# Kernel optimization log

Hardware: AMD Instinct MI355X
Metric: run time of the kernel (lower is better)

The kernel has to match this reference:

```python
import jax, jax.numpy as jnp
import numpy as np

NEG_INF = -10000.0
ALPHA = 0.2      # LeakyReLU slope
EPS = 1e-5       # LayerNorm eps
B, N, D = 8, 2048, 128


def setup_inputs() -> dict:
    key = jax.random.key(0)
    ks = jax.random.split(key, 8)
    x = jax.random.normal(ks[0], (B, N, D), dtype=jnp.float32)
    adj_bool = jax.random.randint(ks[1], (B, N, N), 0, 2, dtype=jnp.int32)
    node_mask = jax.random.randint(ks[2], (B, N), 0, 2, dtype=jnp.int32)
    s = 1.0 / np.sqrt(D)
    W = jax.random.uniform(ks[3], (D, D), jnp.float32, -s, s)    # fc weight (in->out)
    a_l = jax.random.uniform(ks[4], (D,), jnp.float32, -s, s)    # attn_l weight
    a_r = jax.random.uniform(ks[5], (D,), jnp.float32, -s, s)    # attn_r weight
    gamma = jnp.ones((D,), jnp.float32)                          # LayerNorm weight
    beta = jnp.zeros((D,), jnp.float32)                          # LayerNorm bias
    return {"x": x, "adj_bool": adj_bool, "node_mask": node_mask,
            "W": W, "a_l": a_l, "a_r": a_r, "gamma": gamma, "beta": beta}


def reference(x, adj_bool, node_mask, W, a_l, a_r, gamma, beta):
    m = node_mask.astype(x.dtype)[..., None]           # [B,N,1]
    x = x * m
    h = jnp.einsum('bnd,de->bne', x, W)                # [B,N,D]
    e_l = jnp.einsum('bnd,d->bn', h, a_l)              # [B,N]
    e_r = jnp.einsum('bnd,d->bn', h, a_r)              # [B,N]
    e = e_l[:, :, None] + e_r[:, None, :]              # [B,N,N]
    e = jnp.where(e > 0, e, ALPHA * e)                 # LeakyReLU
    pair = (node_mask[:, :, None] * node_mask[:, None, :]) > 0
    allowed = (adj_bool > 0) & pair
    e = jnp.where(allowed, e, NEG_INF)
    attn = jax.nn.softmax(e, axis=-1)                  # finite (NEG_INF fill), nan_to_num is a no-op
    out = jnp.einsum('bij,bjd->bid', attn, h)          # dropout in eval mode = identity
    out = (out + x) * m                                # residual (ind==outd), then node mask
    mu = jnp.mean(out, axis=-1, keepdims=True)
    var = jnp.var(out, axis=-1, keepdims=True)
    out = (out - mu) * jax.lax.rsqrt(var + EPS) * gamma + beta
    return out
```

## Files before the change

kernel.cpp:

```cpp
#include <hip/hip_runtime.h>
#include <stdint.h>


#define BB 8
#define NN 2048
#define DD 128
#define LN_EPS 1e-5f

typedef __attribute__((ext_vector_type(8))) short short8;
typedef __attribute__((ext_vector_type(4))) float f32x4;

__device__ __forceinline__ unsigned pk_bf16(float a, float b) {
    unsigned ua = __float_as_uint(a); ua += 0x7FFFu + ((ua >> 16) & 1u);
    unsigned ub = __float_as_uint(b); ub += 0x7FFFu + ((ub >> 16) & 1u);
    return (ua >> 16) | (ub & 0xFFFF0000u);
}

__global__ __launch_bounds__(256) void wprep_kernel(
    const float* __restrict__ W, unsigned* __restrict__ WT2g)
{
    const int g  = blockIdx.x * 256 + threadIdx.x;
    const int e  = g & 127;
    const int kp = g >> 7;
    const float w0 = W[(size_t)(2 * kp) * DD + e];
    const float w1 = W[(size_t)(2 * kp + 1) * DD + e];
    WT2g[((size_t)(kp >> 2) * 128 + e) * 4 + (kp & 3)] = pk_bf16(w0, w1);
}

__global__ __launch_bounds__(256) void pack_kernel(
    const int* __restrict__ adj, const int* __restrict__ mask,
    unsigned* __restrict__ adjw)
{
    const int t  = threadIdx.x;
    const int w  = t >> 6, ln = t & 63;
    const int r  = blockIdx.x * 4 + w;
    const int b  = r >> 11;
    const int4* arow4 = (const int4*)(adj + (size_t)r * NN);
    const int4* mrow4 = (const int4*)(mask + ((size_t)b << 11));

    unsigned myword = 0;
#pragma unroll
    for (int c = 0; c < 8; ++c) {
        int4 a = arow4[c * 64 + ln];
        int4 m = mrow4[c * 64 + ln];
        unsigned nib = (unsigned)(a.x & m.x & 1)
                     | ((unsigned)(a.y & m.y & 1) << 1)
                     | ((unsigned)(a.z & m.z & 1) << 2)
                     | ((unsigned)(a.w & m.w & 1) << 3);
        unsigned v = nib << ((ln & 7) * 4);
        v |= __shfl_xor(v, 1, 64);
        v |= __shfl_xor(v, 2, 64);
        v |= __shfl_xor(v, 4, 64);
        unsigned got = __shfl(v, (ln & 7) * 8, 64);
        if ((ln >> 3) == c) myword = got;
    }
    adjw[(size_t)r * 64 + ln] = myword;
}

__global__ __launch_bounds__(256) void fc_kernel(
    const float* __restrict__ x, const int* __restrict__ mask,
    const unsigned* __restrict__ WT2g, const float* __restrict__ a_l,
    const float* __restrict__ a_r, unsigned short* __restrict__ hTX,
    float* __restrict__ el, float* __restrict__ er)
{
    __shared__ __align__(16) unsigned char smem[41984];

    const int t   = threadIdx.x;
    const int blk = blockIdx.x;
    const int b   = blk >> 6;
    const int it  = blk & 63;
    const int i0  = it * 32;
    const int half = it & 1;
    const int jt   = it >> 1;

    unsigned short* WT2 = (unsigned short*)smem;
    unsigned* xs2u = (unsigned*)(smem + 32768);
    unsigned* hws  = (unsigned*)(smem + 32768);

    {
        uint4* d = (uint4*)WT2;
        const uint4* s = (const uint4*)WT2g;
#pragma unroll
        for (int k = 0; k < 8; ++k) d[t + 256 * k] = s[t + 256 * k];
    }

    {
#pragma unroll
        for (int s4 = 0; s4 < 4; ++s4) {
            int idx = t + 256 * s4;
            int i = idx >> 5, c4 = idx & 31;
            float4 f = *(const float4*)(x + ((size_t)(b * NN + i0 + i)) * DD
                                          + c4 * 4);
            float mm = (float)mask[b * NN + i0 + i];
            unsigned p0 = pk_bf16(f.x * mm, f.y * mm);
            unsigned p1 = pk_bf16(f.z * mm, f.w * mm);
            unsigned* dst = xs2u + ((size_t)((c4 >> 1) * 32 + i)) * 4
                          + (c4 & 1) * 2;
            dst[0] = p0; dst[1] = p1;
        }
    }
    __syncthreads();

    const int lane = t & 63, w = t >> 6;
    const int row = lane & 15, grp = lane >> 4;

    f32x4 acc[2][2];
#pragma unroll
    for (int mt = 0; mt < 2; ++mt)
#pragma unroll
        for (int nt = 0; nt < 2; ++nt) acc[mt][nt] = (f32x4)0.f;

#pragma unroll
    for (int kk = 0; kk < 4; ++kk) {
        const unsigned short* cb = WT2 + ((size_t)(kk * 4 + grp) * 128) * 8;
        short8 A0 = *(const short8*)(cb + (w * 32 + row) * 8);
        short8 A1 = *(const short8*)(cb + (w * 32 + 16 + row) * 8);
        const unsigned short* xb = (const unsigned short*)xs2u
                                 + ((size_t)(kk * 4 + grp) * 32) * 8;
#pragma unroll
        for (int nt = 0; nt < 2; ++nt) {
            short8 Bv = *(const short8*)(xb + (nt * 16 + row) * 8);
            acc[0][nt] = __builtin_amdgcn_mfma_f32_16x16x32_bf16(A0, Bv, acc[0][nt], 0, 0, 0);
            acc[1][nt] = __builtin_amdgcn_mfma_f32_16x16x32_bf16(A1, Bv, acc[1][nt], 0, 0, 0);
        }
    }
    __syncthreads();

    float al8[2][4], ar8[2][4];
#pragma unroll
    for (int mt = 0; mt < 2; ++mt)
#pragma unroll
        for (int reg = 0; reg < 4; ++reg) {
            int e = w * 32 + mt * 16 + grp * 4 + reg;
            al8[mt][reg] = a_l[e];
            ar8[mt][reg] = a_r[e];
        }
    float* sE = (float*)smem;
#pragma unroll
    for (int nt = 0; nt < 2; ++nt) {
        float pl = 0.f, pr = 0.f;
#pragma unroll
        for (int mt = 0; mt < 2; ++mt)
#pragma unroll
            for (int reg = 0; reg < 4; ++reg) {
                pl += acc[mt][nt][reg] * al8[mt][reg];
                pr += acc[mt][nt][reg] * ar8[mt][reg];
            }
        pl += __shfl_xor(pl, 16, 64); pl += __shfl_xor(pl, 32, 64);
        pr += __shfl_xor(pr, 16, 64); pr += __shfl_xor(pr, 32, 64);
        if (grp == 0) {
            sE[w * 32 + nt * 16 + row]       = pl;
            sE[128 + w * 32 + nt * 16 + row] = pr;
        }
    }

    unsigned* hw = hws + w * 576;
#pragma unroll
    for (int mt = 0; mt < 2; ++mt)
#pragma unroll
        for (int nt = 0; nt < 2; ++nt)
#pragma unroll
            for (int reg = 0; reg < 4; ++reg) {
                float v  = acc[mt][nt][reg];
                float vp = __shfl_xor(v, 1, 64);
                if ((row & 1) == 0)
                    hw[(mt * 16 + grp * 4 + reg) * 18 + ((nt * 16 + row) >> 1)] =
                        pk_bf16(v, vp);
            }
    {
        const int dl = lane & 31, part = lane >> 5;
        unsigned short* dstb = hTX + (size_t)b * (DD * NN) + (size_t)jt * 8192;
#pragma unroll
        for (int pp = 0; pp < 2; ++pp) {
            int ic2 = part * 2 + pp;
            uint4 q = *(const uint4*)(hw + dl * 18 + ic2 * 4);
            *(uint4*)(dstb + ((size_t)((half * 4 + ic2) * 128 + w * 32 + dl)) * 8) = q;
        }
    }

    __syncthreads();
    if (t < 32)
        el[b * NN + i0 + t] = sE[t] + sE[32 + t] + sE[64 + t] + sE[96 + t];
    else if (t < 64) {
        int i = t - 32;
        er[b * NN + i0 + i] = sE[128 + i] + sE[160 + i] + sE[192 + i] + sE[224 + i];
    }
}

__global__ __launch_bounds__(256, 4) void attn_kernel(
    const float* __restrict__ x, const unsigned* __restrict__ adjw,
    const int* __restrict__ mask, const unsigned short* __restrict__ hTX,
    const float* __restrict__ el, const float* __restrict__ er,
    const float* __restrict__ gamma, const float* __restrict__ beta,
    float* __restrict__ outp)
{
    __shared__ __align__(16) float sAcc[4][16][132];
    __shared__ float sL[4][16];

    const int t    = threadIdx.x;
    const int w    = t >> 6;
    const int lane = t & 63;
    const int row  = lane & 15;
    const int grp  = lane >> 4;
    const int b    = blockIdx.x >> 7;
    const int it   = blockIdx.x & 127;
    const int i0   = it * 16;
    const int gi   = i0 + row;

    const float el_r = el[b * NN + gi];
    const int   mi   = mask[b * NN + gi];
    const unsigned* aw_row = adjw + ((size_t)(b * NN + gi)) * 64;
    const float* er_b = er + b * NN;
    const unsigned short* hTX_b = hTX + (size_t)b * DD * NN;

    f32x4 acc[8];
#pragma unroll
    for (int nb = 0; nb < 8; ++nb) acc[nb] = (f32x4)0.f;
    float l_lane = 0.f;

    const int jt0  = w * 8;
    const int voff = (grp * 128 + row) * 8;

    union BU { int4 q; short8 v; };
    union AU { unsigned u[4]; short8 v; };

#pragma unroll 1
    for (int jj = 0; jj < 8; ++jj) {
        const int jt = jt0 + jj;
        const uint2 wv = *(const uint2*)(aw_row + jt * 2);
        const unsigned w0 = mi ? wv.x : 0u;
        const unsigned w1 = mi ? wv.y : 0u;
        const int jb = jt * 64 + grp * 8;
        const unsigned short* hp = hTX_b + (size_t)jt * 8192 + voff;

        {
            BU bf[8];
#pragma unroll
            for (int nb = 0; nb < 8; ++nb)
                bf[nb].q = *(const int4*)(hp + nb * 128);
            const float4 e0 = *(const float4*)(er_b + jb);
            const float4 e1 = *(const float4*)(er_b + jb + 4);
            const float ev[8] = {e0.x,e0.y,e0.z,e0.w, e1.x,e1.y,e1.z,e1.w};
            float p[8];
#pragma unroll
            for (int u = 0; u < 8; ++u) {
                float s = el_r + ev[u];
                s = fmaxf(s, 0.2f * s);
                p[u] = ((w0 >> (grp * 8 + u)) & 1u) ? __expf(s) : 0.f;
                l_lane += p[u];
            }
            AU A;
#pragma unroll
            for (int k = 0; k < 4; ++k) A.u[k] = pk_bf16(p[2*k], p[2*k+1]);
#pragma unroll
            for (int nb = 0; nb < 8; ++nb)
                acc[nb] = __builtin_amdgcn_mfma_f32_16x16x32_bf16(A.v, bf[nb].v, acc[nb], 0, 0, 0);
        }
        {
            BU bf[8];
#pragma unroll
            for (int nb = 0; nb < 8; ++nb)
                bf[nb].q = *(const int4*)(hp + 4096 + nb * 128);
            const float4 e2 = *(const float4*)(er_b + jb + 32);
            const float4 e3 = *(const float4*)(er_b + jb + 36);
            const float ev[8] = {e2.x,e2.y,e2.z,e2.w, e3.x,e3.y,e3.z,e3.w};
            float p[8];
#pragma unroll
            for (int u = 0; u < 8; ++u) {
                float s = el_r + ev[u];
                s = fmaxf(s, 0.2f * s);
                p[u] = ((w1 >> (grp * 8 + u)) & 1u) ? __expf(s) : 0.f;
                l_lane += p[u];
            }
            AU A;
#pragma unroll
            for (int k = 0; k < 4; ++k) A.u[k] = pk_bf16(p[2*k], p[2*k+1]);
#pragma unroll
            for (int nb = 0; nb < 8; ++nb)
                acc[nb] = __builtin_amdgcn_mfma_f32_16x16x32_bf16(A.v, bf[nb].v, acc[nb], 0, 0, 0);
        }
    }

    l_lane += __shfl_xor(l_lane, 16, 64);
    l_lane += __shfl_xor(l_lane, 32, 64);
    if (grp == 0) sL[w][row] = l_lane;
#pragma unroll
    for (int nb = 0; nb < 8; ++nb)
#pragma unroll
        for (int reg = 0; reg < 4; ++reg)
            sAcc[w][grp * 4 + reg][nb * 16 + row] = acc[nb][reg];
    __syncthreads();

    const int crow = t >> 4;
    const int cl   = t & 15;
    const int gr   = i0 + crow;

    const float Ls   = sL[0][crow] + sL[1][crow] + sL[2][crow] + sL[3][crow];
    const float linv = Ls > 0.f ? 1.0f / Ls : 0.f;
    const float mrow = (float)mask[b * NN + gr];
    const float* xrow = x + ((size_t)(b * NN + gr)) * DD;

    float vbuf[8];
    float s1 = 0.f, s2 = 0.f;
#pragma unroll
    for (int h = 0; h < 2; ++h) {
        const int c0 = cl * 8 + h * 4;
        float4 xv = *(const float4*)(xrow + c0);
        float4 a0 = *(const float4*)(&sAcc[0][crow][c0]);
        float4 a1 = *(const float4*)(&sAcc[1][crow][c0]);
        float4 a2 = *(const float4*)(&sAcc[2][crow][c0]);
        float4 a3 = *(const float4*)(&sAcc[3][crow][c0]);
        float tv;
        tv = ((a0.x + a1.x + a2.x + a3.x) * linv + xv.x) * mrow;
        vbuf[h*4+0] = tv; s1 += tv; s2 += tv*tv;
        tv = ((a0.y + a1.y + a2.y + a3.y) * linv + xv.y) * mrow;
        vbuf[h*4+1] = tv; s1 += tv; s2 += tv*tv;
        tv = ((a0.z + a1.z + a2.z + a3.z) * linv + xv.z) * mrow;
        vbuf[h*4+2] = tv; s1 += tv; s2 += tv*tv;
        tv = ((a0.w + a1.w + a2.w + a3.w) * linv + xv.w) * mrow;
        vbuf[h*4+3] = tv; s1 += tv; s2 += tv*tv;
    }
#pragma unroll
    for (int off = 1; off < 16; off <<= 1) {
        s1 += __shfl_xor(s1, off, 64);
        s2 += __shfl_xor(s2, off, 64);
    }
    const float mu  = s1 * (1.0f / DD);
    const float var = s2 * (1.0f / DD) - mu * mu;
    const float rsd = rsqrtf(var + LN_EPS);

    float* orow = outp + ((size_t)(b * NN + gr)) * DD;
#pragma unroll
    for (int h = 0; h < 2; ++h) {
        const int c0 = cl * 8 + h * 4;
        float4 g  = *(const float4*)(gamma + c0);
        float4 be = *(const float4*)(beta + c0);
        float4 o;
        o.x = (vbuf[h*4+0] - mu) * rsd * g.x + be.x;
        o.y = (vbuf[h*4+1] - mu) * rsd * g.y + be.y;
        o.z = (vbuf[h*4+2] - mu) * rsd * g.z + be.z;
        o.w = (vbuf[h*4+3] - mu) * rsd * g.w + be.w;
        *(float4*)(orow + c0) = o;
    }
}

extern "C" void kernel_launch(void* const* d_in, const int* in_sizes, int n_in,
                              void* d_out, int out_size, void* d_ws, size_t ws_size,
                              hipStream_t stream) {
    const float* x     = (const float*)d_in[0];
    const int*   adj   = (const int*)d_in[1];
    const int*   maskp = (const int*)d_in[2];
    const float* W     = (const float*)d_in[3];
    const float* a_l   = (const float*)d_in[4];
    const float* a_r   = (const float*)d_in[5];
    const float* gamma = (const float*)d_in[6];
    const float* beta  = (const float*)d_in[7];
    float*       outp  = (float*)d_out;

    unsigned short* hTX = (unsigned short*)d_ws;
    float* el = (float*)(hTX + (size_t)BB * DD * NN);
    float* er = el + (size_t)BB * NN;
    unsigned* adjw = (unsigned*)(er + (size_t)BB * NN);
    unsigned* WT2g = adjw + (size_t)BB * NN * 64;

    wprep_kernel<<<32, 256, 0, stream>>>(W, WT2g);
    pack_kernel<<<BB * NN / 4, 256, 0, stream>>>(adj, maskp, adjw);
    fc_kernel<<<BB * (NN / 32), 256, 0, stream>>>(x, maskp, WT2g, a_l, a_r,
                                                  hTX, el, er);
    attn_kernel<<<BB * (NN / 16), 256, 0, stream>>>(x, adjw, maskp, hTX,
                                                    el, er, gamma, beta, outp);
}
```

Baseline: 241.3 us.

## Merge weight prep, adjacency packing and FC into one launch

Three preparatory kernels become a single prep kernel. The first 512 blocks do the FC projection and each converts W to packed bf16 directly into shared memory, while the remaining 4096 blocks pack adjacency bits. This removes two kernel launches and the serial dependency between packing and FC, so the two can overlap on the GPU. In exchange, every FC block now re-reads and converts all of W from global memory, and the packing blocks reserve the same 41 KB of shared memory, which may reduce their occupancy.

```diff
diff --git a/kernel.cpp b/kernel.cpp
--- a/kernel.cpp
+++ b/kernel.cpp
@@ -6,6 +6,9 @@
 #define NN 2048
 #define DD 128
 #define LN_EPS 1e-5f
+
+#define FC_BLOCKS 512
+#define PK_BLOCKS 4096
 
 typedef __attribute__((ext_vector_type(8))) short short8;
 typedef __attribute__((ext_vector_type(4))) float f32x4;
@@ -16,57 +19,45 @@
     return (ua >> 16) | (ub & 0xFFFF0000u);
 }
 
-__global__ __launch_bounds__(256) void wprep_kernel(
-    const float* __restrict__ W, unsigned* __restrict__ WT2g)
-{
-    const int g  = blockIdx.x * 256 + threadIdx.x;
-    const int e  = g & 127;
-    const int kp = g >> 7;
-    const float w0 = W[(size_t)(2 * kp) * DD + e];
-    const float w1 = W[(size_t)(2 * kp + 1) * DD + e];
-    WT2g[((size_t)(kp >> 2) * 128 + e) * 4 + (kp & 3)] = pk_bf16(w0, w1);
-}
-
-__global__ __launch_bounds__(256) void pack_kernel(
-    const int* __restrict__ adj, const int* __restrict__ mask,
-    unsigned* __restrict__ adjw)
-{
-    const int t  = threadIdx.x;
-    const int w  = t >> 6, ln = t & 63;
-    const int r  = blockIdx.x * 4 + w;
-    const int b  = r >> 11;
-    const int4* arow4 = (const int4*)(adj + (size_t)r * NN);
-    const int4* mrow4 = (const int4*)(mask + ((size_t)b << 11));
-
-    unsigned myword = 0;
-#pragma unroll
-    for (int c = 0; c < 8; ++c) {
-        int4 a = arow4[c * 64 + ln];
-        int4 m = mrow4[c * 64 + ln];
-        unsigned nib = (unsigned)(a.x & m.x & 1)
-                     | ((unsigned)(a.y & m.y & 1) << 1)
-                     | ((unsigned)(a.z & m.z & 1) << 2)
-                     | ((unsigned)(a.w & m.w & 1) << 3);
-        unsigned v = nib << ((ln & 7) * 4);
-        v |= __shfl_xor(v, 1, 64);
-        v |= __shfl_xor(v, 2, 64);
-        v |= __shfl_xor(v, 4, 64);
-        unsigned got = __shfl(v, (ln & 7) * 8, 64);
-        if ((ln >> 3) == c) myword = got;
-    }
-    adjw[(size_t)r * 64 + ln] = myword;
-}
-
-__global__ __launch_bounds__(256) void fc_kernel(
+__global__ __launch_bounds__(256) void prep_kernel(
     const float* __restrict__ x, const int* __restrict__ mask,
-    const unsigned* __restrict__ WT2g, const float* __restrict__ a_l,
-    const float* __restrict__ a_r, unsigned short* __restrict__ hTX,
-    float* __restrict__ el, float* __restrict__ er)
+    const float* __restrict__ W, const float* __restrict__ a_l,
+    const float* __restrict__ a_r, const int* __restrict__ adj,
+    unsigned short* __restrict__ hTX, float* __restrict__ el,
+    float* __restrict__ er, unsigned* __restrict__ adjw)
 {
     __shared__ __align__(16) unsigned char smem[41984];
 
     const int t   = threadIdx.x;
     const int blk = blockIdx.x;
+
+    if (blk >= FC_BLOCKS) {
+        const int w  = t >> 6, ln = t & 63;
+        const int r  = (blk - FC_BLOCKS) * 4 + w;
+        const int b  = r >> 11;
+        const int4* arow4 = (const int4*)(adj + (size_t)r * NN);
+        const int4* mrow4 = (const int4*)(mask + ((size_t)b << 11));
+
+        unsigned myword = 0;
+#pragma unroll
+        for (int c = 0; c < 8; ++c) {
+            int4 a = arow4[c * 64 + ln];
+            int4 m = mrow4[c * 64 + ln];
+            unsigned nib = (unsigned)(a.x & m.x & 1)
+                         | ((unsigned)(a.y & m.y & 1) << 1)
+                         | ((unsigned)(a.z & m.z & 1) << 2)
+                         | ((unsigned)(a.w & m.w & 1) << 3);
+            unsigned v = nib << ((ln & 7) * 4);
+            v |= __shfl_xor(v, 1, 64);
+            v |= __shfl_xor(v, 2, 64);
+            v |= __shfl_xor(v, 4, 64);
+            unsigned got = __shfl(v, (ln & 7) * 8, 64);
+            if ((ln >> 3) == c) myword = got;
+        }
+        adjw[(size_t)r * 64 + ln] = myword;
+        return;
+    }
+
     const int b   = blk >> 6;
     const int it  = blk & 63;
     const int i0  = it * 32;
@@ -74,14 +65,18 @@
     const int jt   = it >> 1;
 
     unsigned short* WT2 = (unsigned short*)smem;
+    unsigned* WT2u = (unsigned*)smem;
     unsigned* xs2u = (unsigned*)(smem + 32768);
     unsigned* hws  = (unsigned*)(smem + 32768);
 
-    {
-        uint4* d = (uint4*)WT2;
-        const uint4* s = (const uint4*)WT2g;
-#pragma unroll
-        for (int k = 0; k < 8; ++k) d[t + 256 * k] = s[t + 256 * k];
+#pragma unroll 4
+    for (int s = 0; s < 32; ++s) {
+        int g  = t + 256 * s;
+        int e  = g & 127;
+        int kp = g >> 7;
+        float w0 = W[(size_t)(2 * kp) * DD + e];
+        float w1 = W[(size_t)(2 * kp + 1) * DD + e];
+        WT2u[((kp >> 2) * 128 + e) * 4 + (kp & 3)] = pk_bf16(w0, w1);
     }
 
     {
@@ -361,12 +356,9 @@
     float* el = (float*)(hTX + (size_t)BB * DD * NN);
     float* er = el + (size_t)BB * NN;
     unsigned* adjw = (unsigned*)(er + (size_t)BB * NN);
-    unsigned* WT2g = adjw + (size_t)BB * NN * 64;
-
-    wprep_kernel<<<32, 256, 0, stream>>>(W, WT2g);
-    pack_kernel<<<BB * NN / 4, 256, 0, stream>>>(adj, maskp, adjw);
-    fc_kernel<<<BB * (NN / 32), 256, 0, stream>>>(x, maskp, WT2g, a_l, a_r,
-                                                  hTX, el, er);
+
+    prep_kernel<<<FC_BLOCKS + PK_BLOCKS, 256, 0, stream>>>(
+        x, maskp, W, a_l, a_r, adj, hTX, el, er, adjw);
     attn_kernel<<<BB * (NN / 16), 256, 0, stream>>>(x, adjw, maskp, hTX,
                                                     el, er, gamma, beta, outp);
 }
```

New measurement: 236.8 us. About the same (-1.8%).
